# Kernel optimization log

Measured on AMD Instinct MI355X. Metric: run time of the kernel, lower is better.

Reference implementation:

```python
import jax, jax.numpy as jnp
import numpy as np

NUM_HEADS = 16
HEAD_DIM = 64
INPUT_DIM = 1024
EMBED_DIM = NUM_HEADS * HEAD_DIM  # 1024


def setup_inputs() -> dict:
    key = jax.random.key(0)
    ks = jax.random.split(key, 9)
    B, S = 4, 2048
    scale = 1.0 / np.sqrt(INPUT_DIM)
    return {
        "q": jax.random.normal(ks[0], (B, S, INPUT_DIM), dtype=jnp.float32),
        "k": jax.random.normal(ks[1], (B, S, INPUT_DIM), dtype=jnp.float32),
        "v": jax.random.normal(ks[2], (B, S, INPUT_DIM), dtype=jnp.float32),
        "Wq": jax.random.normal(ks[3], (INPUT_DIM, EMBED_DIM), dtype=jnp.float32) * scale,
        "bq": jax.random.normal(ks[4], (EMBED_DIM,), dtype=jnp.float32) * 0.02,
        "Wk": jax.random.normal(ks[5], (INPUT_DIM, EMBED_DIM), dtype=jnp.float32) * scale,
        "bk": jax.random.normal(ks[6], (EMBED_DIM,), dtype=jnp.float32) * 0.02,
        "Wv": jax.random.normal(ks[7], (INPUT_DIM, EMBED_DIM), dtype=jnp.float32) * scale,
        "bv": jax.random.normal(ks[8], (EMBED_DIM,), dtype=jnp.float32) * 0.02,
    }


def reference(q, k, v, Wq, bq, Wk, bk, Wv, bv):
    B, Sq, _ = q.shape
    Sk = k.shape[1]
    # QKV projections (dropout_prob=0 -> identity; ReLU on value path)
    query = (q @ Wq + bq).reshape(B, Sq, NUM_HEADS, HEAD_DIM).transpose(0, 2, 1, 3)  # [B,H,Sq,D]
    key_ = (k @ Wk + bk).reshape(B, Sk, NUM_HEADS, HEAD_DIM).transpose(0, 2, 1, 3)   # [B,H,Sk,D]
    value = jax.nn.relu(v @ Wv + bv).reshape(B, Sk, NUM_HEADS, HEAD_DIM).transpose(0, 2, 1, 3)
    scores = jnp.einsum("bhqd,bhkd->bhqk", query, key_) / np.sqrt(HEAD_DIM).astype(np.float32)
    p_attn = jax.nn.softmax(scores, axis=-1)
    x = jnp.einsum("bhqk,bhkd->bhqd", p_attn, value)  # [B,H,Sq,D]
    return x.transpose(0, 2, 1, 3).reshape(B, Sq, EMBED_DIM)
```

## Files before the change

### kernel.cpp

```cpp
#include <hip/hip_runtime.h>
#include <hip/hip_bf16.h>
#include <stdint.h>

#define BB    4
#define NH    16
#define SEQ   2048
#define DH    64
#define EMB   1024
#define KD    1024
#define MROWS 8192

typedef short  short8  __attribute__((ext_vector_type(8)));
typedef float  f32x4   __attribute__((ext_vector_type(4)));
typedef float  f32x16  __attribute__((ext_vector_type(16)));

typedef const __attribute__((address_space(1))) void* gas_t;
typedef __attribute__((address_space(3))) void*       las_t;
#define GLD16(g, l) __builtin_amdgcn_global_load_lds((gas_t)(g), (las_t)(l), 16, 0, 0)

__device__ __forceinline__ unsigned short f2bf(float f) {
    unsigned u = __float_as_uint(f);
    u += 0x7fffu + ((u >> 16) & 1u);
    return (unsigned short)(u >> 16);
}
__device__ __forceinline__ unsigned packbf(float lo, float hi) {
    union { __hip_bfloat162 h; unsigned u; } cv;
    cv.h = __float22bfloat162_rn(make_float2(lo, hi));
    return cv.u;
}

__global__ __launch_bounds__(256) void conv_kernel(const float* __restrict__ src,
                                                   unsigned short* __restrict__ dst) {
    const size_t i = ((size_t)blockIdx.x * 256 + threadIdx.x) * 8;
    float4 f0 = *(const float4*)(src + i);
    float4 f1 = *(const float4*)(src + i + 4);
    uint4 u;
    u.x = packbf(f0.x, f0.y); u.y = packbf(f0.z, f0.w);
    u.z = packbf(f1.x, f1.y); u.w = packbf(f1.z, f1.w);
    *(uint4*)(dst + i) = u;
}

__global__ __launch_bounds__(256) void wt_kernel(const float* __restrict__ Wq,
                                                 const float* __restrict__ Wk,
                                                 const float* __restrict__ Wv,
                                                 unsigned short* __restrict__ Wt) {
    __shared__ float tsh[64 * 68];
    const int p = blockIdx.z;
    const float* W = (p == 0) ? Wq : (p == 1) ? Wk : Wv;
    unsigned short* dst = Wt + (size_t)p * (KD * EMB);
    const int k0 = blockIdx.x * 64, n0 = blockIdx.y * 64;
    const int t = threadIdx.x;
    {
        const int r = t >> 2, c4 = (t & 3) * 16;
        const float* g = W + (size_t)(k0 + r) * EMB + n0 + c4;
        float* row = &tsh[r * 68 + c4];
        *(float4*)(row + 0)  = *(const float4*)(g + 0);
        *(float4*)(row + 4)  = *(const float4*)(g + 4);
        *(float4*)(row + 8)  = *(const float4*)(g + 8);
        *(float4*)(row + 12) = *(const float4*)(g + 12);
    }
    __syncthreads();
    {
        const int j = t >> 2, kp = (t & 3) * 16;
        unsigned ub[8];
#pragma unroll
        for (int ii = 0; ii < 8; ++ii)
            ub[ii] = packbf(tsh[(kp + 2 * ii) * 68 + j], tsh[(kp + 2 * ii + 1) * 68 + j]);
        unsigned short* o = dst + (size_t)(n0 + j) * KD + k0 + kp;
        *(uint4*)(o + 0) = uint4{ub[0], ub[1], ub[2], ub[3]};
        *(uint4*)(o + 8) = uint4{ub[4], ub[5], ub[6], ub[7]};
    }
}

__global__ __launch_bounds__(256) void proj_kernel(
    const unsigned short* __restrict__ Abf, const unsigned short* __restrict__ Wp,
    const float* __restrict__ bias, unsigned short* __restrict__ dst, const int mode)
{
    __shared__ __align__(16) unsigned short smem[16640];
    unsigned short* Ash = smem;
    unsigned short* Bsh = smem + 4096;

    const int row0 = blockIdx.x * 128;
    const int col0 = blockIdx.y * 128;
    const int t = threadIdx.x, lane = t & 63, wv = t >> 6;
    const int ln15 = lane & 15, q4 = lane >> 4;
    const int wm = wv & 1, wn = wv >> 1;

    f32x4 acc[4][4];
#pragma unroll
    for (int i = 0; i < 4; ++i)
#pragma unroll
        for (int j = 0; j < 4; ++j)
#pragma unroll
            for (int r = 0; r < 4; ++r) acc[i][j][r] = 0.f;

    const unsigned short* gA0 = Abf + (size_t)(row0 + wv * 32 + (lane >> 2)) * KD + (lane & 3) * 8;
    const unsigned short* gA1 = gA0 + 16 * KD;
    const unsigned short* gB0 = Wp  + (size_t)(col0 + wv * 32 + (lane >> 2)) * KD + (lane & 3) * 8;
    const unsigned short* gB1 = gB0 + 16 * KD;
    unsigned short* lA0 = Ash + wv * 1024;
    unsigned short* lA1 = lA0 + 512;
    unsigned short* lB0 = Bsh + wv * 1024;
    unsigned short* lB1 = lB0 + 512;

    for (int k0 = 0; k0 < KD; k0 += 32) {
        GLD16(gA0 + k0, lA0);
        GLD16(gA1 + k0, lA1);
        GLD16(gB0 + k0, lB0);
        GLD16(gB1 + k0, lB1);
        __syncthreads();

        short8 af[4], bfr[4];
#pragma unroll
        for (int mi = 0; mi < 4; ++mi)
            af[mi] = *(const short8*)&Ash[(wm * 64 + mi * 16 + ln15) * 32 + q4 * 8];
#pragma unroll
        for (int ni = 0; ni < 4; ++ni)
            bfr[ni] = *(const short8*)&Bsh[(wn * 64 + ni * 16 + ln15) * 32 + q4 * 8];
#pragma unroll
        for (int mi = 0; mi < 4; ++mi)
#pragma unroll
            for (int ni = 0; ni < 4; ++ni)
                acc[mi][ni] = __builtin_amdgcn_mfma_f32_16x16x32_bf16(
                    af[mi], bfr[ni], acc[mi][ni], 0, 0, 0);
        __syncthreads();
    }

    float bvv[4];
#pragma unroll
    for (int ni = 0; ni < 4; ++ni) bvv[ni] = bias[col0 + wn * 64 + ni * 16 + ln15];
    const float scq = 0.18033688011112042f;

    if (mode < 2) {
#pragma unroll
        for (int mi = 0; mi < 4; ++mi)
#pragma unroll
            for (int r = 0; r < 4; ++r) {
                const int m = row0 + wm * 64 + mi * 16 + q4 * 4 + r;
                const int bi = m >> 11, s = m & 2047;
#pragma unroll
                for (int ni = 0; ni < 4; ++ni) {
                    const int n = col0 + wn * 64 + ni * 16 + ln15;
                    const int hh = n >> 6, dd = n & 63;
                    float v = acc[mi][ni][r] + bvv[ni];
                    if (mode == 0) v *= scq;
                    dst[((size_t)(bi * NH + hh) * SEQ + s) * DH + dd] = f2bf(v);
                }
            }
    } else {
        unsigned short* Tsh = smem;
#pragma unroll
        for (int mi = 0; mi < 4; ++mi)
#pragma unroll
            for (int ni = 0; ni < 4; ++ni)
#pragma unroll
                for (int r = 0; r < 4; ++r) {
                    const int mr = wm * 64 + mi * 16 + q4 * 4 + r;
                    const int ec = wn * 64 + ni * 16 + ln15;
                    float v = acc[mi][ni][r] + bvv[ni];
                    v = v > 0.f ? v : 0.f;
                    Tsh[mr * 130 + ec] = f2bf(v);
                }
        __syncthreads();
        const int e = t >> 1, sh2 = t & 1;
        const int n = col0 + e, hh = n >> 6, dd = n & 63;
        const int bi = row0 >> 11, sbase = (row0 & 2047) + sh2 * 64;
        unsigned ub[32];
#pragma unroll
        for (int i = 0; i < 32; ++i)
            ub[i] = (unsigned)Tsh[(sh2 * 64 + 2 * i) * 130 + e] |
                    ((unsigned)Tsh[(sh2 * 64 + 2 * i + 1) * 130 + e] << 16);
        unsigned short* o = dst + ((size_t)(bi * NH + hh) * DH + dd) * SEQ + sbase;
#pragma unroll
        for (int c = 0; c < 8; ++c)
            *(uint4*)(o + 8 * c) = uint4{ub[4 * c], ub[4 * c + 1], ub[4 * c + 2], ub[4 * c + 3]};
    }
}

__global__ __launch_bounds__(256) void attn_kernel(
    const unsigned short* __restrict__ Qg, const unsigned short* __restrict__ Kg,
    const unsigned short* __restrict__ Vt, float* __restrict__ out)
{
    __shared__ __align__(16) unsigned char smem[34816];
    unsigned short* Ksh = (unsigned short*)smem;
    unsigned short* Vsh = (unsigned short*)smem + 64 * 72;
    float* Osh = (float*)smem;

    const int qb = blockIdx.x, hh = blockIdx.y, bb = blockIdx.z;
    const int t = threadIdx.x, lane = t & 63, wv = t >> 6;
    const int ln31 = lane & 31, h2 = lane >> 5;
    const size_t bh = (size_t)(bb * NH + hh);
    const unsigned short* Qp = Qg + bh * (SEQ * DH);
    const unsigned short* Kp = Kg + bh * (SEQ * DH);
    const unsigned short* Vp = Vt + bh * (DH * SEQ);
    const int q0 = qb * 128 + wv * 32;

    short8 qf[4];
#pragma unroll
    for (int dc = 0; dc < 4; ++dc)
        qf[dc] = *(const short8*)(Qp + (size_t)(q0 + ln31) * DH + h2 * 8 + dc * 16);

    f32x16 accO[2];
#pragma unroll
    for (int i = 0; i < 16; ++i) { accO[0][i] = 0.f; accO[1][i] = 0.f; }
    float m_run = -INFINITY, l_run = 0.f;

    const int srow = t >> 2, sp = (t & 3) * 16;
    const unsigned short* gk = Kp + (size_t)srow * DH + sp;
    const unsigned short* gv = Vp + (size_t)srow * SEQ + sp;
    unsigned short* lk = &Ksh[srow * 72 + sp];
    unsigned short* lv = &Vsh[srow * 72 + sp];

    for (int kt0 = 0; kt0 < SEQ; kt0 += 64) {
        __syncthreads();
        *(short8*)lk       = *(const short8*)(gk + (size_t)kt0 * DH);
        *(short8*)(lk + 8) = *(const short8*)(gk + (size_t)kt0 * DH + 8);
        *(short8*)lv       = *(const short8*)(gv + kt0);
        *(short8*)(lv + 8) = *(const short8*)(gv + kt0 + 8);
        __syncthreads();

        f32x16 st[2];
#pragma unroll
        for (int kt = 0; kt < 2; ++kt) {
#pragma unroll
            for (int i = 0; i < 16; ++i) st[kt][i] = 0.f;
#pragma unroll
            for (int dc = 0; dc < 4; ++dc) {
                short8 kf = *(const short8*)&Ksh[(kt * 32 + ln31) * 72 + h2 * 8 + dc * 16];
                st[kt] = __builtin_amdgcn_mfma_f32_32x32x16_bf16(kf, qf[dc], st[kt], 0, 0, 0);
            }
        }
        float vmax = -INFINITY;
#pragma unroll
        for (int kt = 0; kt < 2; ++kt)
#pragma unroll
            for (int r = 0; r < 16; ++r) vmax = fmaxf(vmax, st[kt][r]);
        vmax = fmaxf(vmax, __shfl_xor(vmax, 32));
        const float m_new = fmaxf(m_run, vmax);
        const float alpha = __builtin_amdgcn_exp2f(m_run - m_new);
        float ts = 0.f;
#pragma unroll
        for (int kt = 0; kt < 2; ++kt)
#pragma unroll
            for (int r = 0; r < 16; ++r) {
                const float pv = __builtin_amdgcn_exp2f(st[kt][r] - m_new);
                st[kt][r] = pv; ts += pv;
            }
        ts += __shfl_xor(ts, 32);
        l_run = l_run * alpha + ts;
        m_run = m_new;
#pragma unroll
        for (int i = 0; i < 16; ++i) { accO[0][i] *= alpha; accO[1][i] *= alpha; }

#pragma unroll
        for (int kt = 0; kt < 2; ++kt) {
            unsigned ow[8], xw[8];
#pragma unroll
            for (int i = 0; i < 8; ++i) {
                ow[i] = packbf(st[kt][2 * i], st[kt][2 * i + 1]);
                xw[i] = (unsigned)__shfl_xor((int)ow[i], 32);
            }
#pragma unroll
            for (int kc = 0; kc < 2; ++kc) {
                union { unsigned u[4]; short8 v; } pf;
                pf.u[0] = h2 ? xw[4 * kc + 2] : ow[4 * kc + 0];
                pf.u[1] = h2 ? xw[4 * kc + 3] : ow[4 * kc + 1];
                pf.u[2] = h2 ? ow[4 * kc + 2] : xw[4 * kc + 0];
                pf.u[3] = h2 ? ow[4 * kc + 3] : xw[4 * kc + 1];
                const int nc = kt * 2 + kc;
#pragma unroll
                for (int dt = 0; dt < 2; ++dt) {
                    short8 vf = *(const short8*)&Vsh[(dt * 32 + ln31) * 72 + nc * 16 + h2 * 8];
                    accO[dt] = __builtin_amdgcn_mfma_f32_32x32x16_bf16(vf, pf.v, accO[dt], 0, 0, 0);
                }
            }
        }
    }

    const float inv = 1.0f / l_run;
    __syncthreads();
#pragma unroll
    for (int dt = 0; dt < 2; ++dt)
#pragma unroll
        for (int r = 0; r < 16; ++r) {
            const int d = dt * 32 + (r & 3) + 8 * (r >> 2) + 4 * h2;
            Osh[(wv * 32 + ln31) * 68 + d] = accO[dt][r] * inv;
        }
    __syncthreads();
    const int r128 = t >> 1, dh = t & 1;
    float* op = out + (((size_t)(bb * SEQ + qb * 128 + r128) * NH + hh) << 6) + dh * 32;
    const float* osrc = &Osh[r128 * 68 + dh * 32];
#pragma unroll
    for (int c = 0; c < 8; ++c)
        *(float4*)(op + 4 * c) = *(const float4*)(osrc + 4 * c);
}

extern "C" void kernel_launch(void* const* d_in, const int* in_sizes, int n_in,
                              void* d_out, int out_size, void* d_ws, size_t ws_size,
                              hipStream_t stream) {
    const float* qf = (const float*)d_in[0];
    const float* kf = (const float*)d_in[1];
    const float* vf = (const float*)d_in[2];
    const float* Wq = (const float*)d_in[3];
    const float* bq = (const float*)d_in[4];
    const float* Wk = (const float*)d_in[5];
    const float* bk = (const float*)d_in[6];
    const float* Wv = (const float*)d_in[7];
    const float* bv = (const float*)d_in[8];

    char* ws = (char*)d_ws;
    unsigned short* Wt  = (unsigned short*)ws;
    unsigned short* Qg  = (unsigned short*)(ws + 6291456);
    unsigned short* Kg  = Qg + 8388608;
    unsigned short* Vt  = Kg + 8388608;
    unsigned short* Abf = Vt + 8388608;
    float* out = (float*)d_out;

    wt_kernel<<<dim3(16, 16, 3), 256, 0, stream>>>(Wq, Wk, Wv, Wt);

    const float* As[3]   = {qf, kf, vf};
    const float* bs[3]   = {bq, bk, bv};
    unsigned short* ds_[3] = {Qg, Kg, Vt};
    for (int p = 0; p < 3; ++p) {
        conv_kernel<<<4096, 256, 0, stream>>>(As[p], Abf);
        proj_kernel<<<dim3(64, 8), 256, 0, stream>>>(Abf, Wt + (size_t)p * KD * EMB,
                                                     bs[p], ds_[p], p);
    }
    attn_kernel<<<dim3(16, 16, 4), 256, 0, stream>>>(Qg, Kg, Vt, out);
}
```

Before: 365.7 us.

## Batch QKV projections into one launch, swizzle LDS tiles, shrink attention blocks

The three projection GEMMs now run in a single grid with a z dimension. Each input is converted into its own workspace buffer. The GEMM K-step grows from 32 to 64 and uses an XOR-swizzled LDS layout loaded via global_load_lds. The Q and K epilogue is staged through shared memory so it writes coalesced 16-byte stores instead of scattered 2-byte ones. The attention kernel drops to 128 threads per 64 query rows, doubling the grid, and loads K/V tiles directly to LDS with swizzling. The goals are fewer launches, fewer bank conflicts, better store coalescing and more attention occupancy, at the cost of more workspace and more K/V reloads per query.

```diff
diff --git a/kernel.cpp b/kernel.cpp
--- a/kernel.cpp
+++ b/kernel.cpp
@@ -73,12 +73,20 @@
 }
 
 __global__ __launch_bounds__(256) void proj_kernel(
-    const unsigned short* __restrict__ Abf, const unsigned short* __restrict__ Wp,
-    const float* __restrict__ bias, unsigned short* __restrict__ dst, const int mode)
+    const unsigned short* __restrict__ AbfBase, const unsigned short* __restrict__ WtBase,
+    const float* __restrict__ bq, const float* __restrict__ bk, const float* __restrict__ bv,
+    unsigned short* __restrict__ Qg, unsigned short* __restrict__ Kg,
+    unsigned short* __restrict__ Vt)
 {
-    __shared__ __align__(16) unsigned short smem[16640];
+    __shared__ __align__(16) unsigned short smem[17408];
     unsigned short* Ash = smem;
-    unsigned short* Bsh = smem + 4096;
+    unsigned short* Bsh = smem + 8192;
+
+    const int p = blockIdx.z;
+    const unsigned short* Abf = AbfBase + (size_t)p * ((size_t)MROWS * KD);
+    const unsigned short* Wp  = WtBase  + (size_t)p * (KD * EMB);
+    const float* bias = (p == 0) ? bq : (p == 1) ? bk : bv;
+    unsigned short* dst = (p == 0) ? Qg : (p == 1) ? Kg : Vt;
 
     const int row0 = blockIdx.x * 128;
     const int col0 = blockIdx.y * 128;
@@ -94,35 +102,39 @@
 #pragma unroll
             for (int r = 0; r < 4; ++r) acc[i][j][r] = 0.f;
 
-    const unsigned short* gA0 = Abf + (size_t)(row0 + wv * 32 + (lane >> 2)) * KD + (lane & 3) * 8;
-    const unsigned short* gA1 = gA0 + 16 * KD;
-    const unsigned short* gB0 = Wp  + (size_t)(col0 + wv * 32 + (lane >> 2)) * KD + (lane & 3) * 8;
-    const unsigned short* gB1 = gB0 + 16 * KD;
-    unsigned short* lA0 = Ash + wv * 1024;
-    unsigned short* lA1 = lA0 + 512;
-    unsigned short* lB0 = Bsh + wv * 1024;
-    unsigned short* lB1 = lB0 + 512;
-
-    for (int k0 = 0; k0 < KD; k0 += 32) {
-        GLD16(gA0 + k0, lA0);
-        GLD16(gA1 + k0, lA1);
-        GLD16(gB0 + k0, lB0);
-        GLD16(gB1 + k0, lB1);
+    const int lr = lane >> 3, lc = (lane & 7) ^ lr;
+    const unsigned short* gA = Abf + (size_t)(row0 + wv * 32 + lr) * KD + lc * 8;
+    const unsigned short* gB = Wp  + (size_t)(col0 + wv * 32 + lr) * KD + lc * 8;
+    unsigned short* lA = Ash + wv * 32 * 64;
+    unsigned short* lB = Bsh + wv * 32 * 64;
+
+    for (int k0 = 0; k0 < KD; k0 += 64) {
+#pragma unroll
+        for (int i = 0; i < 4; ++i) {
+            GLD16(gA + (size_t)i * 8 * KD + k0, lA + i * 512);
+            GLD16(gB + (size_t)i * 8 * KD + k0, lB + i * 512);
+        }
         __syncthreads();
-
-        short8 af[4], bfr[4];
-#pragma unroll
-        for (int mi = 0; mi < 4; ++mi)
-            af[mi] = *(const short8*)&Ash[(wm * 64 + mi * 16 + ln15) * 32 + q4 * 8];
-#pragma unroll
-        for (int ni = 0; ni < 4; ++ni)
-            bfr[ni] = *(const short8*)&Bsh[(wn * 64 + ni * 16 + ln15) * 32 + q4 * 8];
-#pragma unroll
-        for (int mi = 0; mi < 4; ++mi)
-#pragma unroll
-            for (int ni = 0; ni < 4; ++ni)
-                acc[mi][ni] = __builtin_amdgcn_mfma_f32_16x16x32_bf16(
-                    af[mi], bfr[ni], acc[mi][ni], 0, 0, 0);
+#pragma unroll
+        for (int kk = 0; kk < 2; ++kk) {
+            short8 af[4], bfr[4];
+#pragma unroll
+            for (int mi = 0; mi < 4; ++mi) {
+                const int r = wm * 64 + mi * 16 + ln15;
+                af[mi] = *(const short8*)&Ash[r * 64 + (((kk << 2) | q4) ^ (r & 7)) * 8];
+            }
+#pragma unroll
+            for (int ni = 0; ni < 4; ++ni) {
+                const int r = wn * 64 + ni * 16 + ln15;
+                bfr[ni] = *(const short8*)&Bsh[r * 64 + (((kk << 2) | q4) ^ (r & 7)) * 8];
+            }
+#pragma unroll
+            for (int mi = 0; mi < 4; ++mi)
+#pragma unroll
+                for (int ni = 0; ni < 4; ++ni)
+                    acc[mi][ni] = __builtin_amdgcn_mfma_f32_16x16x32_bf16(
+                        af[mi], bfr[ni], acc[mi][ni], 0, 0, 0);
+        }
         __syncthreads();
     }
 
@@ -131,45 +143,40 @@
     for (int ni = 0; ni < 4; ++ni) bvv[ni] = bias[col0 + wn * 64 + ni * 16 + ln15];
     const float scq = 0.18033688011112042f;
 
-    if (mode < 2) {
-#pragma unroll
-        for (int mi = 0; mi < 4; ++mi)
+    unsigned short* Tsh = smem;
+#pragma unroll
+    for (int mi = 0; mi < 4; ++mi)
+#pragma unroll
+        for (int ni = 0; ni < 4; ++ni)
 #pragma unroll
             for (int r = 0; r < 4; ++r) {
-                const int m = row0 + wm * 64 + mi * 16 + q4 * 4 + r;
-                const int bi = m >> 11, s = m & 2047;
-#pragma unroll
-                for (int ni = 0; ni < 4; ++ni) {
-                    const int n = col0 + wn * 64 + ni * 16 + ln15;
-                    const int hh = n >> 6, dd = n & 63;
-                    float v = acc[mi][ni][r] + bvv[ni];
-                    if (mode == 0) v *= scq;
-                    dst[((size_t)(bi * NH + hh) * SEQ + s) * DH + dd] = f2bf(v);
-                }
-            }
+                const int mr = wm * 64 + mi * 16 + q4 * 4 + r;
+                const int ec = wn * 64 + ni * 16 + ln15;
+                float vv = acc[mi][ni][r] + bvv[ni];
+                if (p == 0) vv *= scq;
+                if (p == 2) vv = vv > 0.f ? vv : 0.f;
+                Tsh[mr * 136 + ec] = f2bf(vv);
+            }
+    __syncthreads();
+
+    if (p < 2) {
+        const int mr = t >> 1, hsel = t & 1;
+        const int m = row0 + mr, bi = m >> 11, s = m & 2047;
+        const int hh = (col0 >> 6) + hsel;
+        const unsigned short* src = &Tsh[mr * 136 + hsel * 64];
+        unsigned short* o = dst + ((size_t)(bi * NH + hh) * SEQ + s) * DH;
+#pragma unroll
+        for (int c = 0; c < 8; ++c)
+            *(uint4*)(o + 8 * c) = *(const uint4*)(src + 8 * c);
     } else {
-        unsigned short* Tsh = smem;
-#pragma unroll
-        for (int mi = 0; mi < 4; ++mi)
-#pragma unroll
-            for (int ni = 0; ni < 4; ++ni)
-#pragma unroll
-                for (int r = 0; r < 4; ++r) {
-                    const int mr = wm * 64 + mi * 16 + q4 * 4 + r;
-                    const int ec = wn * 64 + ni * 16 + ln15;
-                    float v = acc[mi][ni][r] + bvv[ni];
-                    v = v > 0.f ? v : 0.f;
-                    Tsh[mr * 130 + ec] = f2bf(v);
-                }
-        __syncthreads();
         const int e = t >> 1, sh2 = t & 1;
         const int n = col0 + e, hh = n >> 6, dd = n & 63;
         const int bi = row0 >> 11, sbase = (row0 & 2047) + sh2 * 64;
         unsigned ub[32];
 #pragma unroll
         for (int i = 0; i < 32; ++i)
-            ub[i] = (unsigned)Tsh[(sh2 * 64 + 2 * i) * 130 + e] |
-                    ((unsigned)Tsh[(sh2 * 64 + 2 * i + 1) * 130 + e] << 16);
+            ub[i] = (unsigned)Tsh[(sh2 * 64 + 2 * i) * 136 + e] |
+                    ((unsigned)Tsh[(sh2 * 64 + 2 * i + 1) * 136 + e] << 16);
         unsigned short* o = dst + ((size_t)(bi * NH + hh) * DH + dd) * SEQ + sbase;
 #pragma unroll
         for (int c = 0; c < 8; ++c)
@@ -177,13 +184,13 @@
     }
 }
 
-__global__ __launch_bounds__(256) void attn_kernel(
+__global__ __launch_bounds__(128) void attn_kernel(
     const unsigned short* __restrict__ Qg, const unsigned short* __restrict__ Kg,
     const unsigned short* __restrict__ Vt, float* __restrict__ out)
 {
-    __shared__ __align__(16) unsigned char smem[34816];
+    __shared__ __align__(16) unsigned char smem[17408];
     unsigned short* Ksh = (unsigned short*)smem;
-    unsigned short* Vsh = (unsigned short*)smem + 64 * 72;
+    unsigned short* Vsh = (unsigned short*)smem + 4096;
     float* Osh = (float*)smem;
 
     const int qb = blockIdx.x, hh = blockIdx.y, bb = blockIdx.z;
@@ -193,7 +200,7 @@
     const unsigned short* Qp = Qg + bh * (SEQ * DH);
     const unsigned short* Kp = Kg + bh * (SEQ * DH);
     const unsigned short* Vp = Vt + bh * (DH * SEQ);
-    const int q0 = qb * 128 + wv * 32;
+    const int q0 = qb * 64 + wv * 32;
 
     short8 qf[4];
 #pragma unroll
@@ -205,18 +212,19 @@
     for (int i = 0; i < 16; ++i) { accO[0][i] = 0.f; accO[1][i] = 0.f; }
     float m_run = -INFINITY, l_run = 0.f;
 
-    const int srow = t >> 2, sp = (t & 3) * 16;
-    const unsigned short* gk = Kp + (size_t)srow * DH + sp;
-    const unsigned short* gv = Vp + (size_t)srow * SEQ + sp;
-    unsigned short* lk = &Ksh[srow * 72 + sp];
-    unsigned short* lv = &Vsh[srow * 72 + sp];
+    const int lr = lane >> 3, lc = (lane & 7) ^ lr;
+    const unsigned short* gk = Kp + (size_t)(wv * 32 + lr) * DH  + lc * 8;
+    const unsigned short* gv = Vp + (size_t)(wv * 32 + lr) * SEQ + lc * 8;
+    unsigned short* lk = Ksh + wv * 32 * 64;
+    unsigned short* lv = Vsh + wv * 32 * 64;
 
     for (int kt0 = 0; kt0 < SEQ; kt0 += 64) {
         __syncthreads();
-        *(short8*)lk       = *(const short8*)(gk + (size_t)kt0 * DH);
-        *(short8*)(lk + 8) = *(const short8*)(gk + (size_t)kt0 * DH + 8);
-        *(short8*)lv       = *(const short8*)(gv + kt0);
-        *(short8*)(lv + 8) = *(const short8*)(gv + kt0 + 8);
+#pragma unroll
+        for (int i = 0; i < 4; ++i) {
+            GLD16(gk + (size_t)kt0 * DH + (size_t)i * 8 * DH, lk + i * 512);
+            GLD16(gv + kt0 + (size_t)i * 8 * SEQ,             lv + i * 512);
+        }
         __syncthreads();
 
         f32x16 st[2];
@@ -226,7 +234,8 @@
             for (int i = 0; i < 16; ++i) st[kt][i] = 0.f;
 #pragma unroll
             for (int dc = 0; dc < 4; ++dc) {
-                short8 kf = *(const short8*)&Ksh[(kt * 32 + ln31) * 72 + h2 * 8 + dc * 16];
+                const int r = kt * 32 + ln31;
+                short8 kf = *(const short8*)&Ksh[r * 64 + (((dc << 1) | h2) ^ (r & 7)) * 8];
                 st[kt] = __builtin_amdgcn_mfma_f32_32x32x16_bf16(kf, qf[dc], st[kt], 0, 0, 0);
             }
         }
@@ -270,7 +279,8 @@
                 const int nc = kt * 2 + kc;
 #pragma unroll
                 for (int dt = 0; dt < 2; ++dt) {
-                    short8 vf = *(const short8*)&Vsh[(dt * 32 + ln31) * 72 + nc * 16 + h2 * 8];
+                    const int r = dt * 32 + ln31;
+                    short8 vf = *(const short8*)&Vsh[r * 64 + (((nc << 1) | h2) ^ (r & 7)) * 8];
                     accO[dt] = __builtin_amdgcn_mfma_f32_32x32x16_bf16(vf, pf.v, accO[dt], 0, 0, 0);
                 }
             }
@@ -287,9 +297,9 @@
             Osh[(wv * 32 + ln31) * 68 + d] = accO[dt][r] * inv;
         }
     __syncthreads();
-    const int r128 = t >> 1, dh = t & 1;
-    float* op = out + (((size_t)(bb * SEQ + qb * 128 + r128) * NH + hh) << 6) + dh * 32;
-    const float* osrc = &Osh[r128 * 68 + dh * 32];
+    const int r64 = t >> 1, dh = t & 1;
+    float* op = out + (((size_t)(bb * SEQ + qb * 64 + r64) * NH + hh) << 6) + dh * 32;
+    const float* osrc = &Osh[r64 * 68 + dh * 32];
 #pragma unroll
     for (int c = 0; c < 8; ++c)
         *(float4*)(op + 4 * c) = *(const float4*)(osrc + 4 * c);
@@ -313,18 +323,13 @@
     unsigned short* Qg  = (unsigned short*)(ws + 6291456);
     unsigned short* Kg  = Qg + 8388608;
     unsigned short* Vt  = Kg + 8388608;
-    unsigned short* Abf = Vt + 8388608;
+    unsigned short* Ab  = Vt + 8388608;
     float* out = (float*)d_out;
 
     wt_kernel<<<dim3(16, 16, 3), 256, 0, stream>>>(Wq, Wk, Wv, Wt);
-
-    const float* As[3]   = {qf, kf, vf};
-    const float* bs[3]   = {bq, bk, bv};
-    unsigned short* ds_[3] = {Qg, Kg, Vt};
-    for (int p = 0; p < 3; ++p) {
-        conv_kernel<<<4096, 256, 0, stream>>>(As[p], Abf);
-        proj_kernel<<<dim3(64, 8), 256, 0, stream>>>(Abf, Wt + (size_t)p * KD * EMB,
-                                                     bs[p], ds_[p], p);
-    }
-    attn_kernel<<<dim3(16, 16, 4), 256, 0, stream>>>(Qg, Kg, Vt, out);
-}
+    conv_kernel<<<4096, 256, 0, stream>>>(qf, Ab);
+    conv_kernel<<<4096, 256, 0, stream>>>(kf, Ab + 8388608);
+    conv_kernel<<<4096, 256, 0, stream>>>(vf, Ab + 16777216);
+    proj_kernel<<<dim3(64, 8, 3), 256, 0, stream>>>(Ab, Wt, bq, bk, bv, Qg, Kg, Vt);
+    attn_kernel<<<dim3(32, 16, 4), 128, 0, stream>>>(Qg, Kg, Vt, out);
+}
```

Result: slower. 394.1 us (+7.8%).
